# Optimization experiments

Measured on AMD Instinct MI355X. Metric: run time of the kernel, lower is better.

Reference implementation:

```python
import jax, jax.numpy as jnp
import numpy as np

N_NODES = 100_000
SCALAR_DIM = 64
HIDDEN = 64
ATTR_DIM = 3
N_DIH = 1_000_000
IN_DIM = SCALAR_DIM * 2 + ATTR_DIM + 2  # 133
EPS_LN = 1e-5
EPS_NORM = 1e-6


def setup_inputs() -> dict:
    key = jax.random.key(0)
    ks = jax.random.split(key, 8)
    x = jax.random.normal(ks[0], (N_NODES, SCALAR_DIM), jnp.float32)
    pos = jax.random.normal(ks[1], (N_NODES, 3), jnp.float32)
    quadra_index = jax.random.randint(ks[2], (4, N_DIH), 0, N_NODES, jnp.int32)
    quadra_attr = jax.random.normal(ks[3], (N_DIH, ATTR_DIM), jnp.float32)

    def lin(k, fi, fo):
        lim = 1.0 / np.sqrt(fi)
        return jax.random.uniform(k, (fi, fo), jnp.float32, -lim, lim)

    return dict(
        x=x, pos=pos, quadra_index=quadra_index, quadra_attr=quadra_attr,
        ln_gamma=jnp.ones((IN_DIM,), jnp.float32),
        ln_beta=jnp.zeros((IN_DIM,), jnp.float32),
        w1=lin(ks[4], IN_DIM, HIDDEN), b1=jnp.zeros((HIDDEN,), jnp.float32),
        w2=lin(ks[5], HIDDEN, HIDDEN), b2=jnp.zeros((HIDDEN,), jnp.float32),
        w3=lin(ks[6], HIDDEN, SCALAR_DIM), b3=jnp.zeros((SCALAR_DIM,), jnp.float32),
        w_out=jax.random.normal(ks[7], (SCALAR_DIM, SCALAR_DIM), jnp.float32),
    )


def _dihedral_cos_sin(pos, i, j, k, l):
    b1 = pos[j] - pos[i]
    b2 = pos[k] - pos[j]
    b3 = pos[l] - pos[k]
    n1 = jnp.cross(b1, b2)
    n2 = jnp.cross(b2, b3)
    n1 = n1 / jnp.maximum(jnp.linalg.norm(n1, axis=-1, keepdims=True), EPS_NORM)
    n2 = n2 / jnp.maximum(jnp.linalg.norm(n2, axis=-1, keepdims=True), EPS_NORM)
    cos_d = jnp.clip(jnp.sum(n1 * n2, axis=-1), -1.0, 1.0)
    b2n = b2 / jnp.maximum(jnp.linalg.norm(b2, axis=-1, keepdims=True), EPS_NORM)
    m = jnp.cross(n1, b2n)
    sin_d = jnp.sum(m * n2, axis=-1)
    return cos_d, sin_d


def _segment_mean(v, idx, n):
    s = jax.ops.segment_sum(v, idx, num_segments=n)
    c = jax.ops.segment_sum(jnp.ones((idx.shape[0], 1), v.dtype), idx, num_segments=n)
    return s / jnp.maximum(c, 1.0)


def reference(x, pos, quadra_index, quadra_attr,
              ln_gamma, ln_beta, w1, b1, w2, b2, w3, b3, w_out):
    i, j, k, l = quadra_index[0], quadra_index[1], quadra_index[2], quadra_index[3]
    x_scalar = x[:, :SCALAR_DIM]
    cos_d, sin_d = _dihedral_cos_sin(pos, i, j, k, l)
    # [num_dihedrals, 2*scalar_dim + 3 + 2]
    inp = jnp.concatenate(
        [x_scalar[i], x_scalar[l], quadra_attr, cos_d[:, None], sin_d[:, None]], axis=-1)
    # LayerNorm over last dim
    mu = jnp.mean(inp, axis=-1, keepdims=True)
    var = jnp.mean(jnp.square(inp - mu), axis=-1, keepdims=True)
    inp = (inp - mu) * jax.lax.rsqrt(var + EPS_LN) * ln_gamma + ln_beta
    # MLP with SiLU
    h = jax.nn.silu(inp @ w1 + b1)
    h = jax.nn.silu(h @ w2 + b2)
    msg = h @ w3 + b3  # [num_dihedrals, scalar_dim]
    aggr = 0.5 * (_segment_mean(msg, j, N_NODES) + _segment_mean(msg, k, N_NODES))
    # e3nn o3.Linear on scalars: fan-in normalized linear, no bias
    out = (aggr @ w_out) * (1.0 / np.sqrt(SCALAR_DIM))
    return out
```

## Files before the change

### kernel.cpp

```cpp
#include <hip/hip_runtime.h>
#include <math.h>

#define NN 100000
#define ND 1000000
#define INDIM 133
#define K1P 160
#define NCNT (2*NN)
#define SCAN_CHUNK 2048
#define NBLK_SCAN ((NCNT + SCAN_CHUNK - 1) / SCAN_CHUNK)
#define HS 72

typedef __bf16 bf16x8 __attribute__((ext_vector_type(8)));
typedef __bf16 bf16x4 __attribute__((ext_vector_type(4)));
typedef float  f32x4  __attribute__((ext_vector_type(4)));
typedef _Float16 f16;
typedef _Float16 f16x4 __attribute__((ext_vector_type(4)));

__device__ __forceinline__ f32x4 mfma_bf16(bf16x8 a, bf16x8 b, f32x4 c) {
    return __builtin_amdgcn_mfma_f32_16x16x32_bf16(a, b, c, 0, 0, 0);
}

__device__ __forceinline__ float3 f3sub(float3 a, float3 b) {
    return make_float3(a.x - b.x, a.y - b.y, a.z - b.z);
}
__device__ __forceinline__ float3 f3cross(float3 a, float3 b) {
    return make_float3(a.y * b.z - a.z * b.y, a.z * b.x - a.x * b.z, a.x * b.y - a.y * b.x);
}
__device__ __forceinline__ float f3dot(float3 a, float3 b) {
    return a.x * b.x + a.y * b.y + a.z * b.z;
}
__device__ __forceinline__ float3 f3load(const float* __restrict__ p, int idx) {
    const float* q = p + (size_t)idx * 3;
    return make_float3(q[0], q[1], q[2]);
}
__device__ __forceinline__ float fsilu(float v) {
    return v / (1.0f + __expf(-v));
}

__global__ __launch_bounds__(256) void prep_sq(const float* __restrict__ x,
                                               float2* __restrict__ sq) {
    const int n = blockIdx.x * 4 + (threadIdx.x >> 6);
    const int c = threadIdx.x & 63;
    float v = x[(size_t)n * 64 + c];
    float s = v, q = v * v;
#pragma unroll
    for (int d = 1; d < 64; d <<= 1) {
        s += __shfl_xor(s, d);
        q += __shfl_xor(q, d);
    }
    if (c == 0) sq[n] = make_float2(s, q);
}

__global__ __launch_bounds__(256) void prep_all(
    const float* __restrict__ w1, const float* __restrict__ b1,
    const float* __restrict__ w2,
    const float* __restrict__ w3, const float* __restrict__ b3,
    const float* __restrict__ wout,
    const float* __restrict__ gamma, const float* __restrict__ beta,
    __bf16* __restrict__ w1h, __bf16* __restrict__ w1l,
    float* __restrict__ c1, float* __restrict__ d1,
    __bf16* __restrict__ w2h, __bf16* __restrict__ w2l,
    __bf16* __restrict__ w3h, __bf16* __restrict__ w3l,
    float* __restrict__ b3f)
{
    const int b = blockIdx.x, tid = threadIdx.x;
    if (b < 40) {
        int idx = b * 256 + tid;
        int n = idx / K1P, kp = idx - n * K1P;
        float v = (kp < INDIM) ? gamma[kp] * w1[(size_t)kp * 64 + n] : 0.0f;
        __bf16 h = (__bf16)v;
        w1h[idx] = h;
        w1l[idx] = (__bf16)(v - (float)h);
    } else if (b == 40) {
        if (tid < 64) {
            float sc = 0.0f, sd = 0.0f;
            for (int k = 0; k < INDIM; ++k) {
                float wv = w1[(size_t)k * 64 + tid];
                sc = fmaf(gamma[k], wv, sc);
                sd = fmaf(beta[k], wv, sd);
            }
            c1[tid] = sc;
            d1[tid] = sd + b1[tid];
        }
    } else if (b < 57) {
        int idx = (b - 41) * 256 + tid;
        int n = idx >> 6, kp = idx & 63;
        int ko = 16 * (kp & 3) + (kp >> 2);
        float v = w2[(size_t)ko * 64 + n];
        __bf16 h = (__bf16)v;
        w2h[idx] = h;
        w2l[idx] = (__bf16)(v - (float)h);
    } else {
        for (int idx = tid; idx < 64 * 64; idx += 256) {
            int k = idx >> 6, c = idx & 63;
            float s = 0.0f;
            for (int q = 0; q < 64; ++q)
                s = fmaf(w3[(size_t)k * 64 + q], wout[(size_t)q * 64 + c], s);
            s *= 0.0625f;
            __bf16 h = (__bf16)s;
            int kp = 4 * (k & 15) + (k >> 4);
            w3h[(size_t)c * 64 + kp] = h;
            w3l[(size_t)c * 64 + kp] = (__bf16)(s - (float)h);
        }
        if (tid < 64) {
            float s = 0.0f;
            for (int q = 0; q < 64; ++q)
                s = fmaf(b3[q], wout[(size_t)q * 64 + tid], s);
            b3f[tid] = s * 0.0625f;
        }
    }
}

__global__ __launch_bounds__(256) void count_kernel(const int* __restrict__ qidx,
                                                    int* __restrict__ cnt) {
    int e = blockIdx.x * 256 + threadIdx.x;
    if (e < ND) {
        atomicAdd(&cnt[qidx[ND + e]], 1);
        atomicAdd(&cnt[NN + qidx[2 * ND + e]], 1);
    }
}

__global__ __launch_bounds__(256) void scan1(int* data, int* __restrict__ bsum) {
    __shared__ int lds[256];
    const int tid = threadIdx.x;
    const int base = blockIdx.x * SCAN_CHUNK + tid * 8;
    int v[8];
    int tsum = 0;
#pragma unroll
    for (int t = 0; t < 8; ++t) {
        v[t] = (base + t < NCNT) ? data[base + t] : 0;
        tsum += v[t];
    }
    lds[tid] = tsum;
    __syncthreads();
    for (int d = 1; d < 256; d <<= 1) {
        int t = 0;
        if (tid >= d) t = lds[tid - d];
        __syncthreads();
        lds[tid] += t;
        __syncthreads();
    }
    if (tid == 255) bsum[blockIdx.x] = lds[255];
    int run = lds[tid] - tsum;
#pragma unroll
    for (int t = 0; t < 8; ++t) {
        if (base + t < NCNT) data[base + t] = run;
        run += v[t];
    }
}

__global__ __launch_bounds__(128) void scan2(int* __restrict__ bsum) {
    __shared__ int lds[128];
    const int t = threadIdx.x;
    int v = (t < NBLK_SCAN) ? bsum[t] : 0;
    lds[t] = v;
    __syncthreads();
    for (int d = 1; d < 128; d <<= 1) {
        int u = (t >= d) ? lds[t - d] : 0;
        __syncthreads();
        lds[t] += u;
        __syncthreads();
    }
    if (t < NBLK_SCAN) bsum[t] = lds[t] - v;
}

__global__ __launch_bounds__(256) void scan3(int* __restrict__ off,
                                             const int* __restrict__ bsum) {
    const int base = blockIdx.x * SCAN_CHUNK + threadIdx.x * 8;
    const int add = bsum[blockIdx.x];
#pragma unroll
    for (int t = 0; t < 8; ++t) {
        int i = base + t;
        if (i < NCNT) off[i] += add;
    }
}

__global__ __launch_bounds__(256) void fill_kernel(const int* __restrict__ qidx,
                                                   int* __restrict__ off,
                                                   int* __restrict__ slot_j,
                                                   int* __restrict__ slot_k) {
    int e = blockIdx.x * 256 + threadIdx.x;
    if (e < ND) {
        slot_j[e] = atomicAdd(&off[qidx[ND + e]], 1);
        slot_k[e] = atomicAdd(&off[NN + qidx[2 * ND + e]], 1);
    }
}

__global__ __launch_bounds__(256, 3) void edge_mlp_mfma(
    const float* __restrict__ x, const float2* __restrict__ sq,
    const float* __restrict__ pos,
    const int* __restrict__ qidx, const float* __restrict__ qattr,
    const __bf16* __restrict__ w1h, const __bf16* __restrict__ w1l,
    const float* __restrict__ c1, const float* __restrict__ d1,
    const __bf16* __restrict__ w2h, const __bf16* __restrict__ w2l, const float* __restrict__ b2,
    const __bf16* __restrict__ w3h, const __bf16* __restrict__ w3l, const float* __restrict__ b3f,
    const int* __restrict__ slot_j, const int* __restrict__ slot_k,
    f16* __restrict__ msg)
{
    __shared__ __align__(16) __bf16 hsh[4][4][16 * HS];

    const int tid = threadIdx.x;
    const int w   = tid >> 6;
    const int l   = tid & 63;
    const int m   = l & 15;
    const int kg  = l >> 4;
    const int ebase = (blockIdx.x * 4 + w) * 64;
    if (ebase >= ND) return;

    int iA[4], lA[4];
#pragma unroll
    for (int t = 0; t < 4; ++t) {
        const int e = ebase + 16 * t + m;
        iA[t] = qidx[e];
        lA[t] = qidx[3 * ND + e];
    }

    float cosd, sind, at0, at1, at2, se, qe;
    {
        const int e2 = ebase + 16 * kg + m;
        const int i2 = qidx[e2];
        const int j2 = qidx[ND + e2];
        const int k2 = qidx[2 * ND + e2];
        const int l2 = qidx[3 * ND + e2];
        float3 pi = f3load(pos, i2), pj = f3load(pos, j2);
        float3 pk = f3load(pos, k2), pl = f3load(pos, l2);
        float3 d1v_ = f3sub(pj, pi);
        float3 d2v_ = f3sub(pk, pj);
        float3 d3v_ = f3sub(pl, pk);
        float3 n1 = f3cross(d1v_, d2v_);
        float3 n2 = f3cross(d2v_, d3v_);
        float r1 = 1.0f / fmaxf(sqrtf(f3dot(n1, n1)), 1e-6f);
        n1.x *= r1; n1.y *= r1; n1.z *= r1;
        float r2 = 1.0f / fmaxf(sqrtf(f3dot(n2, n2)), 1e-6f);
        n2.x *= r2; n2.y *= r2; n2.z *= r2;
        cosd = fminf(fmaxf(f3dot(n1, n2), -1.0f), 1.0f);
        float rb = 1.0f / fmaxf(sqrtf(f3dot(d2v_, d2v_)), 1e-6f);
        float3 b2n = make_float3(d2v_.x * rb, d2v_.y * rb, d2v_.z * rb);
        float3 mm = f3cross(n1, b2n);
        sind = f3dot(mm, n2);
        at0 = qattr[(size_t)e2 * 3 + 0];
        at1 = qattr[(size_t)e2 * 3 + 1];
        at2 = qattr[(size_t)e2 * 3 + 2];
        se = at0 + at1 + at2 + cosd + sind;
        qe = at0 * at0 + at1 * at1 + at2 * at2 + cosd * cosd + sind * sind;
    }

    bf16x8 ah4[4], al4[4];
    float rs_[4], mn_[4];
#pragma unroll
    for (int t = 0; t < 4; ++t) {
        const int src = m + 16 * t;
        float u4[8] = {__shfl(at0, src), __shfl(at1, src), __shfl(at2, src),
                       __shfl(cosd, src), __shfl(sind, src), 0.f, 0.f, 0.f};
        float g0 = (kg == 0) ? 1.0f : 0.0f;
#pragma unroll
        for (int j = 0; j < 8; ++j) {
            float v = u4[j] * g0;
            __bf16 h = (__bf16)v;
            ah4[t][j] = h;
            al4[t][j] = (__bf16)(v - (float)h);
        }
        float2 si = sq[iA[t]], sl = sq[lA[t]];
        float S = si.x + sl.x + __shfl(se, src);
        float Q = si.y + sl.y + __shfl(qe, src);
        float mu  = S * (1.0f / INDIM);
        float var = Q * (1.0f / INDIM) - mu * mu;
        float rsv = rsqrtf(fmaxf(var, 0.0f) + 1e-5f);
        rs_[t] = rsv;
        mn_[t] = -mu * rsv;
    }

    f32x4 acc[4][4];
#pragma unroll
    for (int t = 0; t < 4; ++t)
#pragma unroll
        for (int nt = 0; nt < 4; ++nt) acc[t][nt] = (f32x4){0.f, 0.f, 0.f, 0.f};

#pragma unroll
    for (int nt = 0; nt < 4; ++nt) {
        const size_t wb = (size_t)(16 * nt + m) * K1P + 128 + 8 * kg;
        bf16x8 bh = *(const bf16x8*)(w1h + wb);
        bf16x8 bl = *(const bf16x8*)(w1l + wb);
#pragma unroll
        for (int t = 0; t < 4; ++t) {
            acc[t][nt] = mfma_bf16(ah4[t], bh, acc[t][nt]);
            acc[t][nt] = mfma_bf16(al4[t], bh, acc[t][nt]);
            acc[t][nt] = mfma_bf16(ah4[t], bl, acc[t][nt]);
        }
    }

#pragma unroll
    for (int s = 0; s < 4; ++s) {
        const int colo = 32 * (s & 1) + 8 * kg;
        bf16x8 ath[4], atl[4];
#pragma unroll
        for (int t = 0; t < 4; ++t) {
            const int r_ = (s < 2) ? iA[t] : lA[t];
            float vv[8];
            *(float4*)&vv[0] = *(const float4*)(x + (size_t)r_ * 64 + colo);
            *(float4*)&vv[4] = *(const float4*)(x + (size_t)r_ * 64 + colo + 4);
#pragma unroll
            for (int j = 0; j < 8; ++j) {
                float v = vv[j];
                __bf16 h = (__bf16)v;
                ath[t][j] = h;
                atl[t][j] = (__bf16)(v - (float)h);
            }
        }
#pragma unroll
        for (int nt = 0; nt < 4; ++nt) {
            const size_t wb = (size_t)(16 * nt + m) * K1P + 32 * s + 8 * kg;
            bf16x8 bh = *(const bf16x8*)(w1h + wb);
            bf16x8 bl = *(const bf16x8*)(w1l + wb);
#pragma unroll
            for (int t = 0; t < 4; ++t) {
                acc[t][nt] = mfma_bf16(ath[t], bh, acc[t][nt]);
                acc[t][nt] = mfma_bf16(atl[t], bh, acc[t][nt]);
                acc[t][nt] = mfma_bf16(ath[t], bl, acc[t][nt]);
            }
        }
    }

    float c1v[4], d1v[4], b2v[4], b3v[4];
#pragma unroll
    for (int nt = 0; nt < 4; ++nt) {
        c1v[nt] = c1[16 * nt + m];
        d1v[nt] = d1[16 * nt + m];
        b2v[nt] = b2[16 * nt + m];
        b3v[nt] = b3f[16 * nt + m];
    }
#pragma unroll
    for (int t = 0; t < 4; ++t) {
        __bf16* hhw = &hsh[w][t][0];
#pragma unroll
        for (int r = 0; r < 4; ++r) {
            float rse = __shfl(rs_[t], 4 * kg + r);
            float mne = __shfl(mn_[t], 4 * kg + r);
            bf16x4 hv4;
#pragma unroll
            for (int nt = 0; nt < 4; ++nt)
                hv4[nt] = (__bf16)fsilu(fmaf(rse, acc[t][nt][r],
                                        fmaf(mne, c1v[nt], d1v[nt])));
            *(bf16x4*)(hhw + (4 * kg + r) * HS + m * 4) = hv4;
        }
    }

    bf16x8 a2h[4][2];
#pragma unroll
    for (int t = 0; t < 4; ++t)
#pragma unroll
        for (int s = 0; s < 2; ++s)
            a2h[t][s] = *(const bf16x8*)(&hsh[w][t][m * HS + 32 * s + 8 * kg]);
    f32x4 acc2[4][4];
#pragma unroll
    for (int t = 0; t < 4; ++t)
#pragma unroll
        for (int nt = 0; nt < 4; ++nt) acc2[t][nt] = (f32x4){0.f, 0.f, 0.f, 0.f};
#pragma unroll
    for (int s = 0; s < 2; ++s) {
#pragma unroll
        for (int nt = 0; nt < 4; ++nt) {
            const size_t wb = (size_t)(16 * nt + m) * 64 + 32 * s + 8 * kg;
            bf16x8 bh = *(const bf16x8*)(w2h + wb);
            bf16x8 bl = *(const bf16x8*)(w2l + wb);
#pragma unroll
            for (int t = 0; t < 4; ++t) {
                acc2[t][nt] = mfma_bf16(a2h[t][s], bh, acc2[t][nt]);
                acc2[t][nt] = mfma_bf16(a2h[t][s], bl, acc2[t][nt]);
            }
        }
    }
#pragma unroll
    for (int t = 0; t < 4; ++t) {
        __bf16* hhw = &hsh[w][t][0];
#pragma unroll
        for (int r = 0; r < 4; ++r) {
            bf16x4 hv4;
#pragma unroll
            for (int nt = 0; nt < 4; ++nt)
                hv4[nt] = (__bf16)fsilu(acc2[t][nt][r] + b2v[nt]);
            *(bf16x4*)(hhw + (4 * kg + r) * HS + m * 4) = hv4;
        }
    }

    bf16x8 a3h[4][2];
#pragma unroll
    for (int t = 0; t < 4; ++t)
#pragma unroll
        for (int s = 0; s < 2; ++s)
            a3h[t][s] = *(const bf16x8*)(&hsh[w][t][m * HS + 32 * s + 8 * kg]);
    f32x4 acc3[4][4];
#pragma unroll
    for (int t = 0; t < 4; ++t)
#pragma unroll
        for (int nt = 0; nt < 4; ++nt) acc3[t][nt] = (f32x4){0.f, 0.f, 0.f, 0.f};
#pragma unroll
    for (int s = 0; s < 2; ++s) {
#pragma unroll
        for (int nt = 0; nt < 4; ++nt) {
            const size_t wb = (size_t)(16 * nt + m) * 64 + 32 * s + 8 * kg;
            bf16x8 bh = *(const bf16x8*)(w3h + wb);
            bf16x8 bl = *(const bf16x8*)(w3l + wb);
#pragma unroll
            for (int t = 0; t < 4; ++t) {
                acc3[t][nt] = mfma_bf16(a3h[t][s], bh, acc3[t][nt]);
                acc3[t][nt] = mfma_bf16(a3h[t][s], bl, acc3[t][nt]);
            }
        }
    }

#pragma unroll
    for (int t = 0; t < 4; ++t) {
#pragma unroll
        for (int r = 0; r < 4; ++r) {
            f16x4 v;
#pragma unroll
            for (int nt = 0; nt < 4; ++nt)
                v[nt] = (f16)(acc3[t][nt][r] + b3v[nt]);
            const int er = ebase + 16 * t + 4 * kg + r;
            *(f16x4*)(msg + (size_t)slot_j[er] * 64 + m * 4) = v;
            *(f16x4*)(msg + (size_t)slot_k[er] * 64 + m * 4) = v;
        }
    }
}

__global__ __launch_bounds__(256) void node_out(const f16* __restrict__ msg,
                                                const int* __restrict__ off,
                                                float* __restrict__ out) {
    const int w   = threadIdx.x >> 6;
    const int l   = threadIdx.x & 63;
    const int sub = l >> 4;
    const int m16 = l & 15;
    for (int n = blockIdx.x * 4 + w; n < NN; n += gridDim.x * 4) {
        int ja = (n == 0) ? 0 : off[n - 1];
        int jb = off[n];
        int ka = off[NN + n - 1];
        int kb = off[NN + n];
        float s0 = 0.f, s1 = 0.f, s2 = 0.f, s3 = 0.f;
        float t0 = 0.f, t1 = 0.f, t2 = 0.f, t3 = 0.f;
        for (int p = ja + sub; p < jb; p += 4) {
            f16x4 v = *(const f16x4*)(msg + (size_t)p * 64 + m16 * 4);
            s0 += (float)v[0]; s1 += (float)v[1];
            s2 += (float)v[2]; s3 += (float)v[3];
        }
        for (int p = ka + sub; p < kb; p += 4) {
            f16x4 v = *(const f16x4*)(msg + (size_t)p * 64 + m16 * 4);
            t0 += (float)v[0]; t1 += (float)v[1];
            t2 += (float)v[2]; t3 += (float)v[3];
        }
        s0 += __shfl_xor(s0, 16); s0 += __shfl_xor(s0, 32);
        s1 += __shfl_xor(s1, 16); s1 += __shfl_xor(s1, 32);
        s2 += __shfl_xor(s2, 16); s2 += __shfl_xor(s2, 32);
        s3 += __shfl_xor(s3, 16); s3 += __shfl_xor(s3, 32);
        t0 += __shfl_xor(t0, 16); t0 += __shfl_xor(t0, 32);
        t1 += __shfl_xor(t1, 16); t1 += __shfl_xor(t1, 32);
        t2 += __shfl_xor(t2, 16); t2 += __shfl_xor(t2, 32);
        t3 += __shfl_xor(t3, 16); t3 += __shfl_xor(t3, 32);
        if (sub == 0) {
            float rj = 1.0f / fmaxf((float)(jb - ja), 1.0f);
            float rk = 1.0f / fmaxf((float)(kb - ka), 1.0f);
            float* o = out + (size_t)n * 64;
            o[m16]      = s0 * rj + t0 * rk;
            o[16 + m16] = s1 * rj + t1 * rk;
            o[32 + m16] = s2 * rj + t2 * rk;
            o[48 + m16] = s3 * rj + t3 * rk;
        }
    }
}


extern "C" void kernel_launch(void* const* d_in, const int* in_sizes, int n_in,
                              void* d_out, int out_size, void* d_ws, size_t ws_size,
                              hipStream_t stream) {
    (void)in_sizes; (void)n_in; (void)out_size;

    const float* x     = (const float*)d_in[0];
    const float* pos   = (const float*)d_in[1];
    const int*   qidx  = (const int*)d_in[2];
    const float* qattr = (const float*)d_in[3];
    const float* gamma = (const float*)d_in[4];
    const float* beta  = (const float*)d_in[5];
    const float* w1    = (const float*)d_in[6];
    const float* b1    = (const float*)d_in[7];
    const float* w2    = (const float*)d_in[8];
    const float* b2    = (const float*)d_in[9];
    const float* w3    = (const float*)d_in[10];
    const float* b3    = (const float*)d_in[11];
    const float* w_out = (const float*)d_in[12];
    float* out = (float*)d_out;

    size_t o = 0;
    auto alloc = [&](size_t bytes) { size_t r = o; o = (o + bytes + 255) & ~(size_t)255; return r; };
    char* W = (char*)d_ws;
    f16*    msg    = (f16*)   (W + alloc((size_t)2 * ND * 64 * sizeof(f16)));
    int*    slot_j = (int*)   (W + alloc((size_t)ND * sizeof(int)));
    int*    slot_k = (int*)   (W + alloc((size_t)ND * sizeof(int)));
    int*    off    = (int*)   (W + alloc((size_t)NCNT * sizeof(int)));
    int*    bsum   = (int*)   (W + alloc((size_t)NBLK_SCAN * sizeof(int)));
    float2* sqt    = (float2*)(W + alloc((size_t)NN * sizeof(float2)));
    __bf16* w1h    = (__bf16*)(W + alloc((size_t)64 * K1P * sizeof(__bf16)));
    __bf16* w1l    = (__bf16*)(W + alloc((size_t)64 * K1P * sizeof(__bf16)));
    __bf16* w2h    = (__bf16*)(W + alloc((size_t)64 * 64 * sizeof(__bf16)));
    __bf16* w2l    = (__bf16*)(W + alloc((size_t)64 * 64 * sizeof(__bf16)));
    __bf16* w3h    = (__bf16*)(W + alloc((size_t)64 * 64 * sizeof(__bf16)));
    __bf16* w3l    = (__bf16*)(W + alloc((size_t)64 * 64 * sizeof(__bf16)));
    float*  c1     = (float*) (W + alloc((size_t)64 * sizeof(float)));
    float*  d1     = (float*) (W + alloc((size_t)64 * sizeof(float)));
    float*  b3f    = (float*) (W + alloc((size_t)64 * sizeof(float)));
    if (ws_size < o) return;

    prep_sq<<<NN / 4, 256, 0, stream>>>(x, sqt);
    prep_all<<<58, 256, 0, stream>>>(w1, b1, w2, w3, b3, w_out, gamma, beta,
                                     w1h, w1l, c1, d1, w2h, w2l, w3h, w3l, b3f);

    hipMemsetAsync(off, 0, (size_t)NCNT * sizeof(int), stream);
    count_kernel<<<(ND + 255) / 256, 256, 0, stream>>>(qidx, off);
    scan1<<<NBLK_SCAN, 256, 0, stream>>>(off, bsum);
    scan2<<<1, 128, 0, stream>>>(bsum);
    scan3<<<NBLK_SCAN, 256, 0, stream>>>(off, bsum);
    fill_kernel<<<(ND + 255) / 256, 256, 0, stream>>>(qidx, off, slot_j, slot_k);

    edge_mlp_mfma<<<(ND / 64 + 3) / 4, 256, 0, stream>>>(x, sqt, pos, qidx, qattr,
                                                         w1h, w1l, c1, d1,
                                                         w2h, w2l, b2, w3h, w3l, b3f,
                                                         slot_j, slot_k, msg);
    node_out<<<4096, 256, 0, stream>>>(msg, off, out);
}
```

Measured before the change: 541.4 us.

## Split CSR counters into per-block-group copies and give each node_out row a quarter-wave

The count and fill atomics now spread across up to four replicated counter arrays, chosen by block index, to cut atomic contention on hot nodes. The scan interleaves these copies per node, so the last copy ends up holding each node's end offset. node_out now gives each node a 16-lane group that walks the j and k segments together, with no cross-lane shuffle reduction. In exchange there is more memset, scan traffic and workspace, and lanes diverge when segment lengths differ.

```diff
diff --git a/kernel.cpp b/kernel.cpp
--- a/kernel.cpp
+++ b/kernel.cpp
@@ -112,40 +112,59 @@
 }
 
 __global__ __launch_bounds__(256) void count_kernel(const int* __restrict__ qidx,
-                                                    int* __restrict__ cnt) {
+                                                    int* __restrict__ cur, int NS) {
     int e = blockIdx.x * 256 + threadIdx.x;
     if (e < ND) {
-        atomicAdd(&cnt[qidx[ND + e]], 1);
-        atomicAdd(&cnt[NN + qidx[2 * ND + e]], 1);
-    }
-}
-
-__global__ __launch_bounds__(256) void scan1(int* data, int* __restrict__ bsum) {
+        int s = blockIdx.x & (NS - 1);
+        atomicAdd(&cur[s * NCNT + qidx[ND + e]], 1);
+        atomicAdd(&cur[s * NCNT + NN + qidx[2 * ND + e]], 1);
+    }
+}
+
+__global__ __launch_bounds__(256) void scan1(int* __restrict__ cur,
+                                             int* __restrict__ bsum, int NS) {
     __shared__ int lds[256];
     const int tid = threadIdx.x;
     const int base = blockIdx.x * SCAN_CHUNK + tid * 8;
-    int v[8];
+    int c[8][4];
+    int tot[8];
     int tsum = 0;
 #pragma unroll
     for (int t = 0; t < 8; ++t) {
-        v[t] = (base + t < NCNT) ? data[base + t] : 0;
-        tsum += v[t];
+        const int i = base + t;
+        tot[t] = 0;
+#pragma unroll
+        for (int s = 0; s < 4; ++s) {
+            c[t][s] = (s < NS && i < NCNT) ? cur[s * NCNT + i] : 0;
+            tot[t] += c[t][s];
+        }
+        tsum += tot[t];
     }
     lds[tid] = tsum;
     __syncthreads();
     for (int d = 1; d < 256; d <<= 1) {
-        int t = 0;
-        if (tid >= d) t = lds[tid - d];
+        int u = 0;
+        if (tid >= d) u = lds[tid - d];
         __syncthreads();
-        lds[tid] += t;
+        lds[tid] += u;
         __syncthreads();
     }
     if (tid == 255) bsum[blockIdx.x] = lds[255];
     int run = lds[tid] - tsum;
 #pragma unroll
     for (int t = 0; t < 8; ++t) {
-        if (base + t < NCNT) data[base + t] = run;
-        run += v[t];
+        const int i = base + t;
+        if (i < NCNT) {
+            int p = run;
+#pragma unroll
+            for (int s = 0; s < 4; ++s) {
+                if (s < NS) {
+                    cur[s * NCNT + i] = p;
+                    p += c[t][s];
+                }
+            }
+            run += tot[t];
+        }
     }
 }
 
@@ -164,25 +183,30 @@
     if (t < NBLK_SCAN) bsum[t] = lds[t] - v;
 }
 
-__global__ __launch_bounds__(256) void scan3(int* __restrict__ off,
-                                             const int* __restrict__ bsum) {
+__global__ __launch_bounds__(256) void scan3(int* __restrict__ cur,
+                                             const int* __restrict__ bsum, int NS) {
     const int base = blockIdx.x * SCAN_CHUNK + threadIdx.x * 8;
     const int add = bsum[blockIdx.x];
 #pragma unroll
     for (int t = 0; t < 8; ++t) {
         int i = base + t;
-        if (i < NCNT) off[i] += add;
+        if (i < NCNT) {
+#pragma unroll
+            for (int s = 0; s < 4; ++s)
+                if (s < NS) cur[s * NCNT + i] += add;
+        }
     }
 }
 
 __global__ __launch_bounds__(256) void fill_kernel(const int* __restrict__ qidx,
-                                                   int* __restrict__ off,
+                                                   int* __restrict__ cur,
                                                    int* __restrict__ slot_j,
-                                                   int* __restrict__ slot_k) {
+                                                   int* __restrict__ slot_k, int NS) {
     int e = blockIdx.x * 256 + threadIdx.x;
     if (e < ND) {
-        slot_j[e] = atomicAdd(&off[qidx[ND + e]], 1);
-        slot_k[e] = atomicAdd(&off[NN + qidx[2 * ND + e]], 1);
+        int s = blockIdx.x & (NS - 1);
+        slot_j[e] = atomicAdd(&cur[s * NCNT + qidx[ND + e]], 1);
+        slot_k[e] = atomicAdd(&cur[s * NCNT + NN + qidx[2 * ND + e]], 1);
     }
 }
 
@@ -425,47 +449,44 @@
 }
 
 __global__ __launch_bounds__(256) void node_out(const f16* __restrict__ msg,
-                                                const int* __restrict__ off,
+                                                const int* __restrict__ endp,
                                                 float* __restrict__ out) {
-    const int w   = threadIdx.x >> 6;
+    const int wv  = threadIdx.x >> 6;
     const int l   = threadIdx.x & 63;
-    const int sub = l >> 4;
+    const int q   = l >> 4;
     const int m16 = l & 15;
-    for (int n = blockIdx.x * 4 + w; n < NN; n += gridDim.x * 4) {
-        int ja = (n == 0) ? 0 : off[n - 1];
-        int jb = off[n];
-        int ka = off[NN + n - 1];
-        int kb = off[NN + n];
-        float s0 = 0.f, s1 = 0.f, s2 = 0.f, s3 = 0.f;
-        float t0 = 0.f, t1 = 0.f, t2 = 0.f, t3 = 0.f;
-        for (int p = ja + sub; p < jb; p += 4) {
-            f16x4 v = *(const f16x4*)(msg + (size_t)p * 64 + m16 * 4);
+    const int n = blockIdx.x * 16 + wv * 4 + q;
+    if (n >= NN) return;
+
+    const int ja = (n == 0) ? 0 : endp[n - 1];
+    const int jb = endp[n];
+    const int ka = endp[NN + n - 1];
+    const int kb = endp[NN + n];
+    const int dj = jb - ja, dk = kb - ka;
+    const int dm = (dj > dk) ? dj : dk;
+
+    float s0 = 0.f, s1 = 0.f, s2 = 0.f, s3 = 0.f;
+    float t0 = 0.f, t1 = 0.f, t2 = 0.f, t3 = 0.f;
+#pragma unroll 2
+    for (int it = 0; it < dm; ++it) {
+        if (it < dj) {
+            f16x4 v = *(const f16x4*)(msg + (size_t)(ja + it) * 64 + m16 * 4);
             s0 += (float)v[0]; s1 += (float)v[1];
             s2 += (float)v[2]; s3 += (float)v[3];
         }
-        for (int p = ka + sub; p < kb; p += 4) {
-            f16x4 v = *(const f16x4*)(msg + (size_t)p * 64 + m16 * 4);
+        if (it < dk) {
+            f16x4 v = *(const f16x4*)(msg + (size_t)(ka + it) * 64 + m16 * 4);
             t0 += (float)v[0]; t1 += (float)v[1];
             t2 += (float)v[2]; t3 += (float)v[3];
         }
-        s0 += __shfl_xor(s0, 16); s0 += __shfl_xor(s0, 32);
-        s1 += __shfl_xor(s1, 16); s1 += __shfl_xor(s1, 32);
-        s2 += __shfl_xor(s2, 16); s2 += __shfl_xor(s2, 32);
-        s3 += __shfl_xor(s3, 16); s3 += __shfl_xor(s3, 32);
-        t0 += __shfl_xor(t0, 16); t0 += __shfl_xor(t0, 32);
-        t1 += __shfl_xor(t1, 16); t1 += __shfl_xor(t1, 32);
-        t2 += __shfl_xor(t2, 16); t2 += __shfl_xor(t2, 32);
-        t3 += __shfl_xor(t3, 16); t3 += __shfl_xor(t3, 32);
-        if (sub == 0) {
-            float rj = 1.0f / fmaxf((float)(jb - ja), 1.0f);
-            float rk = 1.0f / fmaxf((float)(kb - ka), 1.0f);
-            float* o = out + (size_t)n * 64;
-            o[m16]      = s0 * rj + t0 * rk;
-            o[16 + m16] = s1 * rj + t1 * rk;
-            o[32 + m16] = s2 * rj + t2 * rk;
-            o[48 + m16] = s3 * rj + t3 * rk;
-        }
-    }
+    }
+    const float rj = 1.0f / fmaxf((float)dj, 1.0f);
+    const float rk = 1.0f / fmaxf((float)dk, 1.0f);
+    float* o = out + (size_t)n * 64;
+    o[m16]      = s0 * rj + t0 * rk;
+    o[16 + m16] = s1 * rj + t1 * rk;
+    o[32 + m16] = s2 * rj + t2 * rk;
+    o[48 + m16] = s3 * rj + t3 * rk;
 }
 
 
@@ -495,7 +516,6 @@
     f16*    msg    = (f16*)   (W + alloc((size_t)2 * ND * 64 * sizeof(f16)));
     int*    slot_j = (int*)   (W + alloc((size_t)ND * sizeof(int)));
     int*    slot_k = (int*)   (W + alloc((size_t)ND * sizeof(int)));
-    int*    off    = (int*)   (W + alloc((size_t)NCNT * sizeof(int)));
     int*    bsum   = (int*)   (W + alloc((size_t)NBLK_SCAN * sizeof(int)));
     float2* sqt    = (float2*)(W + alloc((size_t)NN * sizeof(float2)));
     __bf16* w1h    = (__bf16*)(W + alloc((size_t)64 * K1P * sizeof(__bf16)));
@@ -507,22 +527,25 @@
     float*  c1     = (float*) (W + alloc((size_t)64 * sizeof(float)));
     float*  d1     = (float*) (W + alloc((size_t)64 * sizeof(float)));
     float*  b3f    = (float*) (W + alloc((size_t)64 * sizeof(float)));
-    if (ws_size < o) return;
+    int NS = 4;
+    while (NS > 1 && o + (size_t)NS * NCNT * sizeof(int) > ws_size) NS >>= 1;
+    int* cur = (int*)(W + o);
+    if (ws_size < o + (size_t)NS * NCNT * sizeof(int)) return;
 
     prep_sq<<<NN / 4, 256, 0, stream>>>(x, sqt);
     prep_all<<<58, 256, 0, stream>>>(w1, b1, w2, w3, b3, w_out, gamma, beta,
                                      w1h, w1l, c1, d1, w2h, w2l, w3h, w3l, b3f);
 
-    hipMemsetAsync(off, 0, (size_t)NCNT * sizeof(int), stream);
-    count_kernel<<<(ND + 255) / 256, 256, 0, stream>>>(qidx, off);
-    scan1<<<NBLK_SCAN, 256, 0, stream>>>(off, bsum);
+    hipMemsetAsync(cur, 0, (size_t)NS * NCNT * sizeof(int), stream);
+    count_kernel<<<(ND + 255) / 256, 256, 0, stream>>>(qidx, cur, NS);
+    scan1<<<NBLK_SCAN, 256, 0, stream>>>(cur, bsum, NS);
     scan2<<<1, 128, 0, stream>>>(bsum);
-    scan3<<<NBLK_SCAN, 256, 0, stream>>>(off, bsum);
-    fill_kernel<<<(ND + 255) / 256, 256, 0, stream>>>(qidx, off, slot_j, slot_k);
+    scan3<<<NBLK_SCAN, 256, 0, stream>>>(cur, bsum, NS);
+    fill_kernel<<<(ND + 255) / 256, 256, 0, stream>>>(qidx, cur, slot_j, slot_k, NS);
 
     edge_mlp_mfma<<<(ND / 64 + 3) / 4, 256, 0, stream>>>(x, sqt, pos, qidx, qattr,
                                                          w1h, w1l, c1, d1,
                                                          w2h, w2l, b2, w3h, w3l, b3f,
                                                          slot_j, slot_k, msg);
-    node_out<<<4096, 256, 0, stream>>>(msg, off, out);
-}
+    node_out<<<(NN + 15) / 16, 256, 0, stream>>>(msg, cur + (size_t)(NS - 1) * NCNT, out);
+}
```

Measured after the change: 563.6 us. 1.04x slower.

## Merge prep kernels with count pass and shrink edge MLP LDS footprint

Applied to the files above, without the earlier changes.

Folds prep_sq, prep_all and count_kernel into one launch that dispatches on block index, removing two kernel launches and their gaps. In edge_mlp_mfma, each wave now reuses one 16-row LDS tile per sub-tile instead of holding four, cutting shared memory per block fourfold. The launch bound rises from 3 to 4 blocks per SIMD-unit. The tradeoff is that store and reload now interleave per tile, and the tighter register budget may cause spills.

```diff
diff --git a/kernel.cpp b/kernel.cpp
--- a/kernel.cpp
+++ b/kernel.cpp
@@ -9,6 +9,8 @@
 #define SCAN_CHUNK 2048
 #define NBLK_SCAN ((NCNT + SCAN_CHUNK - 1) / SCAN_CHUNK)
 #define HS 72
+#define NBLK_X (NN / 4)
+#define NBLK_E ((ND + 255) / 256)
 
 typedef __bf16 bf16x8 __attribute__((ext_vector_type(8)));
 typedef __bf16 bf16x4 __attribute__((ext_vector_type(4)));
@@ -37,31 +39,21 @@
     return v / (1.0f + __expf(-v));
 }
 
-__global__ __launch_bounds__(256) void prep_sq(const float* __restrict__ x,
-                                               float2* __restrict__ sq) {
-    const int n = blockIdx.x * 4 + (threadIdx.x >> 6);
-    const int c = threadIdx.x & 63;
-    float v = x[(size_t)n * 64 + c];
-    float s = v, q = v * v;
-#pragma unroll
-    for (int d = 1; d < 64; d <<= 1) {
-        s += __shfl_xor(s, d);
-        q += __shfl_xor(q, d);
-    }
-    if (c == 0) sq[n] = make_float2(s, q);
-}
-
-__global__ __launch_bounds__(256) void prep_all(
+__global__ __launch_bounds__(256) void prep_merged(
+    const float* __restrict__ x,
     const float* __restrict__ w1, const float* __restrict__ b1,
     const float* __restrict__ w2,
     const float* __restrict__ w3, const float* __restrict__ b3,
     const float* __restrict__ wout,
     const float* __restrict__ gamma, const float* __restrict__ beta,
+    const int* __restrict__ qidx,
     __bf16* __restrict__ w1h, __bf16* __restrict__ w1l,
     float* __restrict__ c1, float* __restrict__ d1,
     __bf16* __restrict__ w2h, __bf16* __restrict__ w2l,
     __bf16* __restrict__ w3h, __bf16* __restrict__ w3l,
-    float* __restrict__ b3f)
+    float* __restrict__ b3f,
+    float2* __restrict__ sq,
+    int* __restrict__ cnt)
 {
     const int b = blockIdx.x, tid = threadIdx.x;
     if (b < 40) {
@@ -90,7 +82,7 @@
         __bf16 h = (__bf16)v;
         w2h[idx] = h;
         w2l[idx] = (__bf16)(v - (float)h);
-    } else {
+    } else if (b == 57) {
         for (int idx = tid; idx < 64 * 64; idx += 256) {
             int k = idx >> 6, c = idx & 63;
             float s = 0.0f;
@@ -108,15 +100,23 @@
                 s = fmaf(b3[q], wout[(size_t)q * 64 + tid], s);
             b3f[tid] = s * 0.0625f;
         }
-    }
-}
-
-__global__ __launch_bounds__(256) void count_kernel(const int* __restrict__ qidx,
-                                                    int* __restrict__ cnt) {
-    int e = blockIdx.x * 256 + threadIdx.x;
-    if (e < ND) {
-        atomicAdd(&cnt[qidx[ND + e]], 1);
-        atomicAdd(&cnt[NN + qidx[2 * ND + e]], 1);
+    } else if (b < 58 + NBLK_X) {
+        const int n = (b - 58) * 4 + (tid >> 6);
+        const int c = tid & 63;
+        float v = x[(size_t)n * 64 + c];
+        float s = v, q = v * v;
+#pragma unroll
+        for (int d = 1; d < 64; d <<= 1) {
+            s += __shfl_xor(s, d);
+            q += __shfl_xor(q, d);
+        }
+        if (c == 0) sq[n] = make_float2(s, q);
+    } else {
+        int e = (b - 58 - NBLK_X) * 256 + tid;
+        if (e < ND) {
+            atomicAdd(&cnt[qidx[ND + e]], 1);
+            atomicAdd(&cnt[NN + qidx[2 * ND + e]], 1);
+        }
     }
 }
 
@@ -134,10 +134,10 @@
     lds[tid] = tsum;
     __syncthreads();
     for (int d = 1; d < 256; d <<= 1) {
-        int t = 0;
-        if (tid >= d) t = lds[tid - d];
+        int u = 0;
+        if (tid >= d) u = lds[tid - d];
         __syncthreads();
-        lds[tid] += t;
+        lds[tid] += u;
         __syncthreads();
     }
     if (tid == 255) bsum[blockIdx.x] = lds[255];
@@ -186,8 +186,9 @@
     }
 }
 
-__global__ __launch_bounds__(256, 3) void edge_mlp_mfma(
-    const float* __restrict__ x, const float2* __restrict__ sq,
+__global__ __launch_bounds__(256, 4) void edge_mlp_mfma(
+    const float* __restrict__ x,
+    const float2* __restrict__ sq,
     const float* __restrict__ pos,
     const int* __restrict__ qidx, const float* __restrict__ qattr,
     const __bf16* __restrict__ w1h, const __bf16* __restrict__ w1l,
@@ -197,7 +198,7 @@
     const int* __restrict__ slot_j, const int* __restrict__ slot_k,
     f16* __restrict__ msg)
 {
-    __shared__ __align__(16) __bf16 hsh[4][4][16 * HS];
+    __shared__ __align__(16) __bf16 hsh[4][16 * HS];
 
     const int tid = threadIdx.x;
     const int w   = tid >> 6;
@@ -329,9 +330,10 @@
         b2v[nt] = b2[16 * nt + m];
         b3v[nt] = b3f[16 * nt + m];
     }
+    __bf16* hhw = &hsh[w][0];
+    bf16x8 a2h[4][2];
 #pragma unroll
     for (int t = 0; t < 4; ++t) {
-        __bf16* hhw = &hsh[w][t][0];
 #pragma unroll
         for (int r = 0; r < 4; ++r) {
             float rse = __shfl(rs_[t], 4 * kg + r);
@@ -343,14 +345,11 @@
                                         fmaf(mne, c1v[nt], d1v[nt])));
             *(bf16x4*)(hhw + (4 * kg + r) * HS + m * 4) = hv4;
         }
-    }
-
-    bf16x8 a2h[4][2];
-#pragma unroll
-    for (int t = 0; t < 4; ++t)
 #pragma unroll
         for (int s = 0; s < 2; ++s)
-            a2h[t][s] = *(const bf16x8*)(&hsh[w][t][m * HS + 32 * s + 8 * kg]);
+            a2h[t][s] = *(const bf16x8*)(hhw + m * HS + 32 * s + 8 * kg);
+    }
+
     f32x4 acc2[4][4];
 #pragma unroll
     for (int t = 0; t < 4; ++t)
@@ -370,9 +369,10 @@
             }
         }
     }
+
+    bf16x8 a3h[4][2];
 #pragma unroll
     for (int t = 0; t < 4; ++t) {
-        __bf16* hhw = &hsh[w][t][0];
 #pragma unroll
         for (int r = 0; r < 4; ++r) {
             bf16x4 hv4;
@@ -381,14 +381,11 @@
                 hv4[nt] = (__bf16)fsilu(acc2[t][nt][r] + b2v[nt]);
             *(bf16x4*)(hhw + (4 * kg + r) * HS + m * 4) = hv4;
         }
-    }
-
-    bf16x8 a3h[4][2];
-#pragma unroll
-    for (int t = 0; t < 4; ++t)
 #pragma unroll
         for (int s = 0; s < 2; ++s)
-            a3h[t][s] = *(const bf16x8*)(&hsh[w][t][m * HS + 32 * s + 8 * kg]);
+            a3h[t][s] = *(const bf16x8*)(hhw + m * HS + 32 * s + 8 * kg);
+    }
+
     f32x4 acc3[4][4];
 #pragma unroll
     for (int t = 0; t < 4; ++t)
@@ -509,20 +506,19 @@
     float*  b3f    = (float*) (W + alloc((size_t)64 * sizeof(float)));
     if (ws_size < o) return;
 
-    prep_sq<<<NN / 4, 256, 0, stream>>>(x, sqt);
-    prep_all<<<58, 256, 0, stream>>>(w1, b1, w2, w3, b3, w_out, gamma, beta,
-                                     w1h, w1l, c1, d1, w2h, w2l, w3h, w3l, b3f);
-
     hipMemsetAsync(off, 0, (size_t)NCNT * sizeof(int), stream);
-    count_kernel<<<(ND + 255) / 256, 256, 0, stream>>>(qidx, off);
+    prep_merged<<<58 + NBLK_X + NBLK_E, 256, 0, stream>>>(
+        x, w1, b1, w2, w3, b3, w_out, gamma, beta, qidx,
+        w1h, w1l, c1, d1, w2h, w2l, w3h, w3l, b3f, sqt, off);
+
     scan1<<<NBLK_SCAN, 256, 0, stream>>>(off, bsum);
     scan2<<<1, 128, 0, stream>>>(bsum);
     scan3<<<NBLK_SCAN, 256, 0, stream>>>(off, bsum);
-    fill_kernel<<<(ND + 255) / 256, 256, 0, stream>>>(qidx, off, slot_j, slot_k);
-
-    edge_mlp_mfma<<<(ND / 64 + 3) / 4, 256, 0, stream>>>(x, sqt, pos, qidx, qattr,
-                                                         w1h, w1l, c1, d1,
-                                                         w2h, w2l, b2, w3h, w3l, b3f,
-                                                         slot_j, slot_k, msg);
+    fill_kernel<<<NBLK_E, 256, 0, stream>>>(qidx, off, slot_j, slot_k);
+
+    edge_mlp_mfma<<<(ND / 64 + 3) / 4, 256, 0, stream>>>(
+        x, sqt, pos, qidx, qattr, w1h, w1l, c1, d1,
+        w2h, w2l, b2, w3h, w3l, b3f, slot_j, slot_k, msg);
+
     node_out<<<4096, 256, 0, stream>>>(msg, off, out);
 }
```

Measured after the change: 556.4 us. +2.8%, slower.
